# Kernel tuning notes

Hardware: AMD Instinct MI355X
Metric: run time of the kernel (lower is better)

Reference implementation:

```python
import jax, jax.numpy as jnp
import numpy as np

N = 262144   # cohort size (k_n)
M = 8192     # number of ordinal anchor indices (len(Hj))


def setup_inputs() -> dict:
    key = jax.random.key(0)
    k1, k2, k3, k4, k5 = jax.random.split(key, 5)
    time = jax.random.uniform(k1, (N,), dtype=jnp.float32) * 1000.0
    event = (jax.random.uniform(k2, (N,), dtype=jnp.float32) < 0.3).astype(jnp.float32)
    y_true0 = jnp.stack([time, event], axis=1)          # [N,2] (time, event)
    y_true1 = y_true0                                    # second head labels (unused by loss)
    y_pred0 = jax.random.normal(k3, (N, 1), dtype=jnp.float32) * 0.1  # xbeta head 0
    y_pred1 = jax.random.normal(k4, (N, 1), dtype=jnp.float32) * 0.1  # xbeta head 1
    Hj = jnp.sort(jax.random.randint(k5, (M,), 0, N, dtype=jnp.int32))  # static event indices into sorted order
    log_vars = jnp.zeros((2, 1), dtype=jnp.float32)      # layer weights log_var0, log_var1
    return {"y_true0": y_true0, "y_true1": y_true1, "y_pred0": y_pred0,
            "y_pred1": y_pred1, "Hj": Hj, "log_vars": log_vars}


def reference(y_true0, y_true1, y_pred0, y_pred1, Hj, log_vars):
    n = y_true0.shape[0]
    # top_k with k = n == full descending sort by time
    _, order = jax.lax.top_k(y_true0[:, 0], n)

    # ---- neg_log_pl (Cox negative partial log-likelihood, per-sample vector) ----
    xbeta = y_pred0[order, 0]                 # [N] sorted by descending time
    event = y_true0[order, 1]                 # [N]
    denom = jnp.cumsum(jnp.exp(xbeta))        # risk-set cumulative sum
    lossA = -(event * (xbeta - jnp.log(denom)))  # [N]

    # ---- ordinal_loss0 (pairwise ranking over event indices Hj in sorted order) ----
    # intended math: for each j, for ii >= j: cost += 1 - exp(xbeta[Hj[j]] - xbeta[Hj[ii]])
    xb = y_pred1[order, 0]                    # [N] sorted
    xh = xb[Hj]                               # [M]
    m = Hj.shape[0]
    rec = 1.0 - jnp.exp(xh[:, None] - xh[None, :])   # [M,M] rec[j,ii]
    mask = jnp.triu(jnp.ones((m, m), dtype=bool))    # ii >= j
    cost2 = jnp.sum(jnp.where(mask, rec, 0.0))

    # ---- multi_loss combination with learned log variances ----
    lv0 = log_vars[0, 0]
    lv1 = log_vars[1, 0]
    precision1 = jnp.clip(jnp.exp(-lv1), 0.0, 1.0)
    loss = jnp.sum(lossA + lv0) + (precision1 * cost2 + lv1)
    return loss


if __name__ == "__main__":
    out = reference(**setup_inputs())
    print(out)
```

## Files before the change

### kernel.cpp

```cpp
#include <hip/hip_runtime.h>
#include <math.h>


#define BSHIFT 12
#define NBUCK (1 << 19)
#define BLK 256
#define NC1 32
#define M40 ((1ull << 40) - 1)

#define STORE_U32(p, v) __hip_atomic_store((p), (v), __ATOMIC_RELAXED, __HIP_MEMORY_SCOPE_AGENT)
#define STORE_F32(p, v) __hip_atomic_store((p), (v), __ATOMIC_RELAXED, __HIP_MEMORY_SCOPE_AGENT)
#define STORE_U64(p, v) __hip_atomic_store((unsigned long long*)(p), (v), __ATOMIC_RELAXED, __HIP_MEMORY_SCOPE_AGENT)

template <int GRID>
__device__ __forceinline__ void gbar(unsigned* bar, unsigned gv) {
  __syncthreads();
  if (threadIdx.x == 0) {
    constexpr unsigned BPC = GRID / NC1;
    const unsigned grp = blockIdx.x & (NC1 - 1);
    unsigned a = __hip_atomic_fetch_add(bar + grp * 16, 1u,
                                        __ATOMIC_RELAXED, __HIP_MEMORY_SCOPE_AGENT);
    if (a == gv * BPC - 1u) {
      unsigned b = __hip_atomic_fetch_add(bar + 512, 1u,
                                          __ATOMIC_RELAXED, __HIP_MEMORY_SCOPE_AGENT);
      if (b == gv * NC1 - 1u) {
        #pragma unroll
        for (int i = 0; i < NC1; ++i)
          STORE_U32(bar + 544 + i * 16, gv);
      }
    }
    int guard = 0;
    while (__hip_atomic_load(bar + 544 + grp * 16, __ATOMIC_RELAXED,
                             __HIP_MEMORY_SCOPE_AGENT) < gv) {
      __builtin_amdgcn_s_sleep(1);
      if (++guard > 2000000) break;
    }
  }
  __syncthreads();
}

template <int GRID>
__global__ void __launch_bounds__(BLK, 4)
k_fused(const float2* __restrict__ yt0, const float* __restrict__ yp0,
        const float* __restrict__ yp1, const int* __restrict__ Hj,
        const float* __restrict__ lv, int n, int m,
        unsigned* __restrict__ bar,
        unsigned long long* __restrict__ rec, unsigned* __restrict__ bitmap,
        uint4* __restrict__ Epack, unsigned* __restrict__ bTot,
        float* __restrict__ fTot, uint2* __restrict__ skey2,
        unsigned* __restrict__ sidx, float* __restrict__ xh,
        double* __restrict__ accum, float* __restrict__ out)
{
  constexpr int TOT = GRID * BLK;
  constexpr int BPB = NBUCK / GRID;
  constexpr int BPT = BPB / BLK;
  const int t = threadIdx.x;
  const int g = blockIdx.x;
  const int gtid = g * BLK + t;

  __shared__ unsigned su[BLK];
  __shared__ float    sff[BLK];
  __shared__ double   sd[BLK];
  __shared__ float    wt[4];

  unsigned keyR[2]; float seR[2]; unsigned seqR[2]; unsigned evR[2];
  #pragma unroll
  for (int el = 0; el < 2; ++el) {
    int i = gtid + el * TOT;
    keyR[el] = 0u; seR[el] = 0.f; seqR[el] = 0u; evR[el] = 0u;
    if (i < n) {
      float2 te = yt0[i];
      unsigned key = __float_as_uint(te.x);
      keyR[el] = key;
      evR[el] = (te.y != 0.f) ? 0x80000000u : 0u;
      float e = expf(yp0[i]);
      seR[el] = e;
      unsigned long long qe = (unsigned long long)(e * 16777216.0f + 0.5f);
      if (qe > (1ull << 32)) qe = (1ull << 32);
      unsigned long long ret =
          atomicAdd(&rec[key >> BSHIFT], (1ull << 40) | qe);
      seqR[el] = (unsigned)(ret >> 40);
    }
  }
  for (int j = gtid; j < m; j += TOT) {
    int h = Hj[j];
    atomicOr(&bitmap[h >> 5], 1u << (h & 31));
  }
  gbar<GRID>(bar, 1);

  unsigned cK[BPT]; float fK[BPT];
  unsigned thrC; float thrF;
  {
    unsigned runc = 0u; float runf = 0.f;
    #pragma unroll
    for (int k = 0; k < BPT; ++k) {
      int b = NBUCK - 1 - (g * BPB + t * BPT + k);
      unsigned long long v = rec[b];
      cK[k] = (unsigned)(v >> 40);
      fK[k] = (float)((double)(v & M40) * (1.0 / 16777216.0));
      runc += cK[k]; runf += fK[k];
    }
    su[t] = runc; sff[t] = runf;
    __syncthreads();
    for (int off2 = 1; off2 < BLK; off2 <<= 1) {
      unsigned uc = (t >= off2) ? su[t - off2] : 0u;
      float    uf = (t >= off2) ? sff[t - off2] : 0.f;
      __syncthreads();
      su[t] += uc; sff[t] += uf;
      __syncthreads();
    }
    thrC = (t > 0) ? su[t - 1] : 0u;
    thrF = (t > 0) ? sff[t - 1] : 0.f;
    if (t == BLK - 1) { STORE_U32(&bTot[g], su[t]); STORE_F32(&fTot[g], sff[t]); }
  }
  gbar<GRID>(bar, 2);

  {
    unsigned partC = 0u; float partF = 0.f;
    for (int j = t; j < g; j += BLK) { partC += bTot[j]; partF += fTot[j]; }
    su[t] = partC; sff[t] = partF;
    __syncthreads();
    for (int s = BLK / 2; s > 0; s >>= 1) {
      if (t < s) { su[t] += su[t + s]; sff[t] += sff[t + s]; }
      __syncthreads();
    }
    unsigned baseC = su[0]; float baseF = sff[0];
    __syncthreads();
    unsigned preC = 0u; float preF = 0.f;
    #pragma unroll
    for (int k = 0; k < BPT; ++k) {
      int b = NBUCK - 1 - (g * BPB + t * BPT + k);
      unsigned sfxC = baseC + thrC + preC;
      float    sfxF = baseF + thrF + preF;
      unsigned long long w =
          ((unsigned long long)__float_as_uint(sfxF) << 32) | sfxC;
      STORE_U64(&Epack[b].x, w);
      STORE_U32(&Epack[b].z, cK[k]);
      preC += cK[k]; preF += fK[k];
    }
  }
  gbar<GRID>(bar, 3);

  #pragma unroll
  for (int el = 0; el < 2; ++el) {
    int i = gtid + el * TOT;
    if (i < n) {
      unsigned key = keyR[el];
      unsigned b = key >> BSHIFT;
      unsigned start = Epack[b].x;
      unsigned pos = start + seqR[el];
      unsigned long long v =
          ((unsigned long long)__float_as_uint(seR[el]) << 32) | key;
      STORE_U64(&skey2[pos], v);
      STORE_U32(&sidx[pos], (unsigned)i | evR[el]);
    }
  }
  gbar<GRID>(bar, 4);

  {
    double contrib = 0.0;
    #pragma unroll
    for (int el = 0; el < 2; ++el) {
      int i = gtid + el * TOT;
      if (i >= n) continue;
      unsigned key = keyR[el];
      float e = seR[el];
      unsigned idx = (unsigned)i;
      bool evb = evR[el] != 0u;
      unsigned b = key >> BSHIFT;
      uint4 ep = Epack[b];
      unsigned start = ep.x;
      float cross = __uint_as_float(ep.y);
      unsigned end = start + ep.z;
      if (end > (unsigned)n) end = (unsigned)n;
      if (start > end) start = end;
      float wsum = 0.f;
      unsigned wcnt = 0u;
      unsigned q = start;
      while (q + 8 <= end) {
        uint2 v[8];
        #pragma unroll
        for (int k = 0; k < 8; ++k) v[k] = skey2[q + k];
        #pragma unroll
        for (int k = 0; k < 8; ++k) {
          if (v[k].x > key) { wsum += __uint_as_float(v[k].y); wcnt++; }
          else if (v[k].x == key && (sidx[q + k] & 0x7FFFFFFFu) < idx) {
            wsum += __uint_as_float(v[k].y); wcnt++;
          }
        }
        q += 8;
      }
      for (; q < end; ++q) {
        uint2 v = skey2[q];
        if (v.x > key) { wsum += __uint_as_float(v.y); wcnt++; }
        else if (v.x == key && (sidx[q] & 0x7FFFFFFFu) < idx) {
          wsum += __uint_as_float(v.y); wcnt++;
        }
      }
      float denom = cross + wsum + e;
      int rank = (int)(start + wcnt);
      if (evb) contrib += (double)logf(denom / e);
      if ((bitmap[rank >> 5] >> (rank & 31)) & 1u) {
        int lo = 0, hi = m;
        while (lo < hi) { int mid = (lo + hi) >> 1; if (Hj[mid] < rank) lo = mid + 1; else hi = mid; }
        if (lo < m && Hj[lo] == rank) {
          float xb1 = yp1[idx];
          for (int j = lo; j < m && Hj[j] == rank; ++j) STORE_F32(&xh[j], xb1);
        }
      }
    }
    sd[t] = contrib;
    __syncthreads();
    for (int s = 128; s > 0; s >>= 1) { if (t < s) sd[t] += sd[t + s]; __syncthreads(); }
    if (t == 0) atomicAdd(accum, sd[0]);
  }
  gbar<GRID>(bar, 5);

  if (g != 0) return;
  {
    int lane = t & 63;
    int w = t >> 6;
    double acc = 0.0;
    float carry = 0.f;
    int passes = (m + 2047) / 2048;
    for (int pss = passes - 1; pss >= 0; --pss) {
      int base = pss * 2048 + t * 8;
      float x[8], eb[8];
      float c = 0.f;
      #pragma unroll
      for (int k = 0; k < 8; ++k) {
        int j = base + k;
        x[k] = (j < m) ? xh[j] : 0.f;
        eb[k] = (j < m) ? expf(-x[k]) : 0.f;
        c += eb[k];
      }
      float s = c;
      #pragma unroll
      for (int d = 1; d < 64; d <<= 1) {
        float o = __shfl_down(s, d, 64);
        if (lane + d < 64) s += o;
      }
      float wtot = __shfl(s, 0, 64);
      if (lane == 0) wt[w] = wtot;
      __syncthreads();
      float after = 0.f, ptot = 0.f;
      #pragma unroll
      for (int w2 = 0; w2 < 4; ++w2) { ptot += wt[w2]; if (w2 > w) after += wt[w2]; }
      float S = (s - c) + after + carry;
      #pragma unroll
      for (int k = 7; k >= 0; --k) {
        int j = base + k;
        S += eb[k];
        if (j < m) acc += (double)(expf(x[k]) * S);
      }
      __syncthreads();
      carry += ptot;
    }
    sd[t] = acc;
    __syncthreads();
    for (int s2 = 128; s2 > 0; s2 >>= 1) { if (t < s2) sd[t] += sd[t + s2]; __syncthreads(); }
    if (t == 0) {
      double T = (double)m * (double)(m + 1) * 0.5;
      double cost2 = T - sd[0];
      float lv0 = lv[0], lv1 = lv[1];
      float prec1 = fminf(expf(-lv1), 1.0f);
      double loss = *accum + (double)n * (double)lv0 + (double)prec1 * cost2 + (double)lv1;
      out[0] = (float)loss;
    }
  }
}

extern "C" void kernel_launch(void* const* d_in, const int* in_sizes, int n_in,
                              void* d_out, int out_size, void* d_ws, size_t ws_size,
                              hipStream_t stream) {
  (void)n_in; (void)out_size;
  const float2* yt0 = (const float2*)d_in[0];
  const float*  yp0 = (const float*)d_in[2];
  const float*  yp1 = (const float*)d_in[3];
  const int*    Hj  = (const int*)d_in[4];
  const float*  lv  = (const float*)d_in[5];
  int n = in_sizes[0] / 2;
  int m = in_sizes[4];

  char* ws = (char*)d_ws;
  unsigned* bar   = (unsigned*)ws;
  double*   accum = (double*)(ws + 6144);
  size_t off = 8192;
  auto alloc = [&](size_t bytes) -> void* {
    void* p = ws + off;
    off += (bytes + 255) & ~(size_t)255;
    return p;
  };
  size_t nbm = ((size_t)(n + 31) / 32) * 4;
  unsigned* bitmap = (unsigned*)alloc(nbm);
  unsigned long long* rec = (unsigned long long*)alloc((size_t)NBUCK * 8);
  size_t zbytes = off;
  uint4*    Epack = (uint4*)alloc((size_t)NBUCK * 16);
  unsigned* bTot  = (unsigned*)alloc(1024 * 4);
  float*    fTot  = (float*)alloc(1024 * 4);
  uint2*    skey2 = (uint2*)alloc((size_t)n * 8);
  unsigned* sidx  = (unsigned*)alloc((size_t)n * 4);
  float*    xh    = (float*)alloc((size_t)m * 4);
  if (off > ws_size) return;

  hipMemsetAsync(ws, 0, zbytes, stream);

  static int gridChoice = 0;
  if (gridChoice == 0) {
    int nb = 0;
    hipError_t e1 = hipOccupancyMaxActiveBlocksPerMultiprocessor(&nb, k_fused<1024>, BLK, 0);
    int dev = 0; hipGetDevice(&dev);
    hipDeviceProp_t prop;
    hipError_t e2 = hipGetDeviceProperties(&prop, dev);
    gridChoice = (e1 == hipSuccess && e2 == hipSuccess &&
                  nb * prop.multiProcessorCount >= 1024) ? 1024 : 512;
  }
  if (gridChoice == 1024)
    k_fused<1024><<<dim3(1024), dim3(BLK), 0, stream>>>(
        yt0, yp0, yp1, Hj, lv, n, m, bar, rec, bitmap, Epack, bTot, fTot,
        skey2, sidx, xh, accum, (float*)d_out);
  else
    k_fused<512><<<dim3(512), dim3(BLK), 0, stream>>>(
        yt0, yp0, yp1, Hj, lv, n, m, bar, rec, bitmap, Epack, bTot, fTot,
        skey2, sidx, xh, accum, (float*)d_out);
}
```

Baseline: 155.3 us.

## Use master-block grid barrier, shrink bucket table, read sorted elements in final pass

The grid barrier changes from a two-level counter tree to one where block 0 polls per-group flags and releases each group through a separate flag, so fewer atomics pile onto a single counter. The bucket table drops from 16 to 8 bytes per entry: the bucket end is now taken from the start offset of the adjacent bucket instead of a stored count. The final pass reads elements in sorted order from skey2/sidx rather than from per-thread registers, so neighbouring threads scan neighbouring buckets with more coalesced access. The cost is extra loads in the last phase and a barrier that depends on block 0 making progress.

```diff
diff --git a/kernel.cpp b/kernel.cpp
--- a/kernel.cpp
+++ b/kernel.cpp
@@ -11,32 +11,42 @@
 #define STORE_U32(p, v) __hip_atomic_store((p), (v), __ATOMIC_RELAXED, __HIP_MEMORY_SCOPE_AGENT)
 #define STORE_F32(p, v) __hip_atomic_store((p), (v), __ATOMIC_RELAXED, __HIP_MEMORY_SCOPE_AGENT)
 #define STORE_U64(p, v) __hip_atomic_store((unsigned long long*)(p), (v), __ATOMIC_RELAXED, __HIP_MEMORY_SCOPE_AGENT)
+#define LOAD_U32(p) __hip_atomic_load((p), __ATOMIC_RELAXED, __HIP_MEMORY_SCOPE_AGENT)
 
 template <int GRID>
 __device__ __forceinline__ void gbar(unsigned* bar, unsigned gv) {
   __syncthreads();
-  if (threadIdx.x == 0) {
-    constexpr unsigned BPC = GRID / NC1;
-    const unsigned grp = blockIdx.x & (NC1 - 1);
-    unsigned a = __hip_atomic_fetch_add(bar + grp * 16, 1u,
-                                        __ATOMIC_RELAXED, __HIP_MEMORY_SCOPE_AGENT);
-    if (a == gv * BPC - 1u) {
-      unsigned b = __hip_atomic_fetch_add(bar + 512, 1u,
+  constexpr unsigned BPC = GRID / NC1;
+  const int t = threadIdx.x;
+  const unsigned grp = blockIdx.x & (NC1 - 1);
+  if (blockIdx.x == 0) {
+    if (t == 0) {
+      unsigned a = __hip_atomic_fetch_add(bar + grp * 16, 1u,
                                           __ATOMIC_RELAXED, __HIP_MEMORY_SCOPE_AGENT);
-      if (b == gv * NC1 - 1u) {
-        #pragma unroll
-        for (int i = 0; i < NC1; ++i)
-          STORE_U32(bar + 544 + i * 16, gv);
-      }
-    }
-    int guard = 0;
-    while (__hip_atomic_load(bar + 544 + grp * 16, __ATOMIC_RELAXED,
-                             __HIP_MEMORY_SCOPE_AGENT) < gv) {
-      __builtin_amdgcn_s_sleep(1);
-      if (++guard > 2000000) break;
-    }
-  }
-  __syncthreads();
+      if (a == gv * BPC - 1u) STORE_U32(bar + 512 + grp * 16, gv);
+    }
+    if (t < NC1) {
+      int guard = 0;
+      while (LOAD_U32(bar + 512 + t * 16) < gv) {
+        __builtin_amdgcn_s_sleep(1);
+        if (++guard > 5000000) break;
+      }
+      STORE_U32(bar + 1024 + t * 16, gv);
+    }
+    __syncthreads();
+  } else {
+    if (t == 0) {
+      unsigned a = __hip_atomic_fetch_add(bar + grp * 16, 1u,
+                                          __ATOMIC_RELAXED, __HIP_MEMORY_SCOPE_AGENT);
+      if (a == gv * BPC - 1u) STORE_U32(bar + 512 + grp * 16, gv);
+      int guard = 0;
+      while (LOAD_U32(bar + 1024 + grp * 16) < gv) {
+        __builtin_amdgcn_s_sleep(1);
+        if (++guard > 5000000) break;
+      }
+    }
+    __syncthreads();
+  }
 }
 
 template <int GRID>
@@ -46,7 +56,7 @@
         const float* __restrict__ lv, int n, int m,
         unsigned* __restrict__ bar,
         unsigned long long* __restrict__ rec, unsigned* __restrict__ bitmap,
-        uint4* __restrict__ Epack, unsigned* __restrict__ bTot,
+        unsigned long long* __restrict__ Epack, unsigned* __restrict__ bTot,
         float* __restrict__ fTot, uint2* __restrict__ skey2,
         unsigned* __restrict__ sidx, float* __restrict__ xh,
         double* __restrict__ accum, float* __restrict__ out)
@@ -134,8 +144,7 @@
       float    sfxF = baseF + thrF + preF;
       unsigned long long w =
           ((unsigned long long)__float_as_uint(sfxF) << 32) | sfxC;
-      STORE_U64(&Epack[b].x, w);
-      STORE_U32(&Epack[b].z, cK[k]);
+      STORE_U64(&Epack[b], w);
       preC += cK[k]; preF += fK[k];
     }
   }
@@ -147,7 +156,7 @@
     if (i < n) {
       unsigned key = keyR[el];
       unsigned b = key >> BSHIFT;
-      unsigned start = Epack[b].x;
+      unsigned start = ((const unsigned*)Epack)[2u * b];
       unsigned pos = start + seqR[el];
       unsigned long long v =
           ((unsigned long long)__float_as_uint(seR[el]) << 32) | key;
@@ -161,17 +170,20 @@
     double contrib = 0.0;
     #pragma unroll
     for (int el = 0; el < 2; ++el) {
-      int i = gtid + el * TOT;
-      if (i >= n) continue;
-      unsigned key = keyR[el];
-      float e = seR[el];
-      unsigned idx = (unsigned)i;
-      bool evb = evR[el] != 0u;
+      int p = gtid + el * TOT;
+      if (p >= n) continue;
+      uint2 kv = skey2[p];
+      unsigned key = kv.x;
+      float e = __uint_as_float(kv.y);
+      unsigned sidv = sidx[p];
+      unsigned idx = sidv & 0x7FFFFFFFu;
+      bool evb = (sidv >> 31) != 0u;
       unsigned b = key >> BSHIFT;
-      uint4 ep = Epack[b];
-      unsigned start = ep.x;
-      float cross = __uint_as_float(ep.y);
-      unsigned end = start + ep.z;
+      unsigned long long ep = Epack[b];
+      unsigned start = (unsigned)ep;
+      float cross = __uint_as_float((unsigned)(ep >> 32));
+      unsigned end = (b > 0) ? ((const unsigned*)Epack)[2u * (b - 1)]
+                             : (unsigned)n;
       if (end > (unsigned)n) end = (unsigned)n;
       if (start > end) start = end;
       float wsum = 0.f;
@@ -284,7 +296,7 @@
 
   char* ws = (char*)d_ws;
   unsigned* bar   = (unsigned*)ws;
-  double*   accum = (double*)(ws + 6144);
+  double*   accum = (double*)(ws + 7168);
   size_t off = 8192;
   auto alloc = [&](size_t bytes) -> void* {
     void* p = ws + off;
@@ -295,7 +307,7 @@
   unsigned* bitmap = (unsigned*)alloc(nbm);
   unsigned long long* rec = (unsigned long long*)alloc((size_t)NBUCK * 8);
   size_t zbytes = off;
-  uint4*    Epack = (uint4*)alloc((size_t)NBUCK * 16);
+  unsigned long long* Epack = (unsigned long long*)alloc((size_t)NBUCK * 8);
   unsigned* bTot  = (unsigned*)alloc(1024 * 4);
   float*    fTot  = (float*)alloc(1024 * 4);
   uint2*    skey2 = (uint2*)alloc((size_t)n * 8);
```

Result: faster. 138.3 us (-10.9%).
